# Performance work log

Measured on AMD Instinct MI355X. Metric: run time of the kernel, lower is better.

Reference implementation:

```python
import jax, jax.numpy as jnp
import numpy as np

N_NODES = 50000


def setup_inputs() -> dict:
    key = jax.random.key(0)
    ks = jax.random.split(key, 10)
    E = 800000
    x = jax.random.normal(ks[0], (N_NODES, 256), dtype=jnp.float32)
    src = jax.random.randint(ks[1], (E,), 0, N_NODES, dtype=jnp.int32)
    dst = jax.random.randint(ks[2], (E,), 0, N_NODES, dtype=jnp.int32)
    w = jax.random.uniform(ks[3], (E,), dtype=jnp.float32)
    W1 = jax.random.normal(ks[4], (256, 128), dtype=jnp.float32) / np.sqrt(256)
    b1 = jnp.zeros((128,), dtype=jnp.float32)
    W2 = jax.random.normal(ks[5], (128, 128), dtype=jnp.float32) / np.sqrt(128)
    b2 = jnp.zeros((128,), dtype=jnp.float32)
    W3 = jax.random.normal(ks[6], (128, 64), dtype=jnp.float32) / np.sqrt(128)
    b3 = jnp.zeros((64,), dtype=jnp.float32)
    return {"x": x, "src": src, "dst": dst, "w": w,
            "W1": W1, "b1": b1, "W2": W2, "b2": b2, "W3": W3, "b3": b3}


def _graph_conv(x, src, dst, w, W, b):
    # dense projection then edge-weighted gather-multiply-scatter-sum
    h = x @ W + b                              # [N, d_out]
    msgs = h[src] * w[:, None]                 # [E, d_out] per-edge messages
    return jax.ops.segment_sum(msgs, dst, num_segments=N_NODES)


def reference(x, src, dst, w, W1, b1, W2, b2, W3, b3):
    h = _graph_conv(x, src, dst, w, W1, b1)
    h = jax.nn.relu(h)
    h = _graph_conv(h, src, dst, w, W2, b2)
    h = jax.nn.relu(h)
    h = _graph_conv(h, src, dst, w, W3, b3)
    return h
```

## Files before the change

### kernel.cpp

```cpp
#include <hip/hip_runtime.h>
#include <hip/hip_bf16.h>

#define N_NODES 50000
#define BSHIFT  6
#define BSIZE   64
#define NBUCK   ((N_NODES + BSIZE - 1) / BSIZE)
#define BIN_BLOCKS 512

using short8  = __attribute__((ext_vector_type(8))) short;
using short4v = __attribute__((ext_vector_type(4))) short;
using floatx4 = __attribute__((ext_vector_type(4))) float;

__device__ inline short f32_to_bf16_bits(float f) {
    __hip_bfloat16 h = __float2bfloat16(f);
    return *reinterpret_cast<short*>(&h);
}

template<int K, int N, bool A_F32>
__global__ __launch_bounds__(256) void mfma_gemm(const void* __restrict__ Araw,
                                                 const short* __restrict__ WTf,
                                                 const float* __restrict__ bias,
                                                 short* __restrict__ C, int M)
{
    constexpr int KS = K / 32;
    constexpr int CT = N / 32;
    constexpr int LK = K + 8;

    __shared__ __align__(16) short As[64][LK];

    const int tid  = threadIdx.x;
    const int wave = tid >> 6;
    const int lane = tid & 63;
    const int l15  = lane & 15;
    const int lk   = (lane >> 4) * 8;
    const int wr   = wave >> 1;
    const int wc   = wave & 1;
    const int r0   = blockIdx.x * 64;

    if (A_F32) {
        const float* Af = (const float*)Araw;
#pragma unroll
        for (int it = 0; it < 64 * (K / 4) / 256; ++it) {
            const int idx = it * 256 + tid;
            const int row = idx / (K / 4);
            const int c4  = idx % (K / 4);
            const int gr  = min(r0 + row, M - 1);
            const float4 v = *reinterpret_cast<const float4*>(&Af[(size_t)gr * K + c4 * 4]);
            short4v s;
            s[0] = f32_to_bf16_bits(v.x); s[1] = f32_to_bf16_bits(v.y);
            s[2] = f32_to_bf16_bits(v.z); s[3] = f32_to_bf16_bits(v.w);
            *reinterpret_cast<short4v*>(&As[row][c4 * 4]) = s;
        }
    } else {
        const short* Ab = (const short*)Araw;
#pragma unroll
        for (int it = 0; it < 64 * (K / 8) / 256; ++it) {
            const int idx = it * 256 + tid;
            const int row = idx / (K / 8);
            const int c8  = idx % (K / 8);
            const int gr  = min(r0 + row, M - 1);
            const short8 v = *reinterpret_cast<const short8*>(&Ab[(size_t)gr * K + c8 * 8]);
            *reinterpret_cast<short8*>(&As[row][c8 * 8]) = v;
        }
    }
    __syncthreads();

    float bv[CT];
#pragma unroll
    for (int t = 0; t < CT; ++t) bv[t] = bias[wc * (N / 2) + t * 16 + l15];

    floatx4 acc[2][CT];
#pragma unroll
    for (int rt = 0; rt < 2; ++rt)
#pragma unroll
        for (int t = 0; t < CT; ++t) acc[rt][t] = (floatx4){0.f, 0.f, 0.f, 0.f};

#pragma unroll
    for (int ks = 0; ks < KS; ++ks) {
        short8 b[CT];
#pragma unroll
        for (int t = 0; t < CT; ++t) {
            const int tg = wc * CT + t;
            b[t] = *reinterpret_cast<const short8*>(&WTf[((size_t)(tg * KS + ks) * 64 + lane) * 8]);
        }
        short8 a[2];
#pragma unroll
        for (int rt = 0; rt < 2; ++rt)
            a[rt] = *reinterpret_cast<const short8*>(&As[wr * 32 + rt * 16 + l15][ks * 32 + lk]);
#pragma unroll
        for (int rt = 0; rt < 2; ++rt)
#pragma unroll
            for (int t = 0; t < CT; ++t)
                acc[rt][t] = __builtin_amdgcn_mfma_f32_16x16x32_bf16(a[rt], b[t], acc[rt][t], 0, 0, 0);
    }

    const int rowg = (lane >> 4) * 4;
#pragma unroll
    for (int rt = 0; rt < 2; ++rt)
#pragma unroll
        for (int t = 0; t < CT; ++t)
#pragma unroll
            for (int j = 0; j < 4; ++j) {
                const int gr = r0 + wr * 32 + rt * 16 + rowg + j;
                if (gr < M)
                    C[(size_t)gr * N + wc * (N / 2) + t * 16 + l15] =
                        f32_to_bf16_bits(acc[rt][t][j] + bv[t]);
            }
}

template<int K, int N>
__global__ __launch_bounds__(256) void fused_pull_gemm(const unsigned int* __restrict__ h,
                                                       const int* __restrict__ row_ptr,
                                                       const unsigned int* __restrict__ csr_ew,
                                                       const short* __restrict__ WTf,
                                                       const float* __restrict__ bias,
                                                       short* __restrict__ C, int M)
{
    static_assert(K == 128, "pull input dim is 128");
    constexpr int KS   = K / 32;
    constexpr int LK   = K + 8;
    constexpr int COLT = N / 32;

    __shared__ __align__(16) short As[32][LK];

    const int tid  = threadIdx.x;
    const int wave = tid >> 6;
    const int lane = tid & 63;
    const int q    = lane >> 4;
    const int l16  = lane & 15;
    const int r0   = blockIdx.x * 32;

#pragma unroll
    for (int rnd = 0; rnd < 2; ++rnd) {
        const int lrow = wave * 8 + rnd * 4 + q;
        const int node = r0 + lrow;
        int beg = 0, end = 0;
        if (node < M) { beg = row_ptr[node]; end = row_ptr[node + 1]; }

        float ax[4][4], ay[4][4];
#pragma unroll
        for (int u = 0; u < 4; ++u)
#pragma unroll
            for (int jj = 0; jj < 4; ++jj) { ax[u][jj] = 0.f; ay[u][jj] = 0.f; }

        unsigned ew = (beg + l16 < end) ? csr_ew[beg + l16] : 0u;
        for (int c = beg; c < end; c += 16) {
            const int nidx = c + 16 + l16;
            const unsigned ew_next = (nidx < end) ? csr_ew[nidx] : 0u;
            const int cnt = min(16, end - c);

            for (int j = 0; j < cnt; j += 8) {
                unsigned e[8];
#pragma unroll
                for (int u = 0; u < 8; ++u) {
                    const unsigned v = __shfl(ew, j + u, 16);
                    e[u] = (j + u < cnt) ? v : 0u;
                }
                uint4 p[8];
#pragma unroll
                for (int u = 0; u < 8; ++u)
                    p[u] = *reinterpret_cast<const uint4*>(&h[(size_t)(e[u] >> 16) * 64 + l16 * 4]);
#pragma unroll
                for (int u = 0; u < 8; ++u) {
                    const float wv = __int_as_float(e[u] << 16);
                    const unsigned* pp = reinterpret_cast<const unsigned*>(&p[u]);
#pragma unroll
                    for (int jj = 0; jj < 4; ++jj) {
                        ax[u & 3][jj] = fmaf(__int_as_float(pp[jj] << 16), wv, ax[u & 3][jj]);
                        ay[u & 3][jj] = fmaf(__int_as_float(pp[jj] & 0xffff0000u), wv, ay[u & 3][jj]);
                    }
                }
            }
            ew = ew_next;
        }

        uint4 o;
        unsigned* ov = reinterpret_cast<unsigned*>(&o);
#pragma unroll
        for (int jj = 0; jj < 4; ++jj) {
            float axs = (ax[0][jj] + ax[1][jj]) + (ax[2][jj] + ax[3][jj]);
            float ays = (ay[0][jj] + ay[1][jj]) + (ay[2][jj] + ay[3][jj]);
            axs = fmaxf(axs, 0.f); ays = fmaxf(ays, 0.f);
            ov[jj] = (unsigned)(unsigned short)f32_to_bf16_bits(axs) |
                     ((unsigned)(unsigned short)f32_to_bf16_bits(ays) << 16);
        }
        *reinterpret_cast<uint4*>(&As[lrow][l16 * 8]) = o;
    }
    __syncthreads();

    const int l15 = lane & 15;
    const int lk  = (lane >> 4) * 8;
    const int wr  = wave >> 1;
    const int wc  = wave & 1;

    float bv[COLT];
#pragma unroll
    for (int t = 0; t < COLT; ++t) bv[t] = bias[wc * (N / 2) + t * 16 + l15];

    floatx4 acc[COLT];
#pragma unroll
    for (int t = 0; t < COLT; ++t) acc[t] = (floatx4){0.f, 0.f, 0.f, 0.f};

#pragma unroll
    for (int ks = 0; ks < KS; ++ks) {
        short8 b[COLT];
#pragma unroll
        for (int t = 0; t < COLT; ++t) {
            const int tg = wc * COLT + t;
            b[t] = *reinterpret_cast<const short8*>(&WTf[((size_t)(tg * KS + ks) * 64 + lane) * 8]);
        }
        const short8 a = *reinterpret_cast<const short8*>(&As[wr * 16 + l15][ks * 32 + lk]);
#pragma unroll
        for (int t = 0; t < COLT; ++t)
            acc[t] = __builtin_amdgcn_mfma_f32_16x16x32_bf16(a, b[t], acc[t], 0, 0, 0);
    }

    const int rowg = (lane >> 4) * 4;
#pragma unroll
    for (int t = 0; t < COLT; ++t)
#pragma unroll
        for (int j = 0; j < 4; ++j) {
            const int gr = r0 + wr * 16 + rowg + j;
            if (gr < M)
                C[(size_t)gr * N + wc * (N / 2) + t * 16 + l15] =
                    f32_to_bf16_bits(acc[t][j] + bv[t]);
        }
}

__device__ inline void wt_frag(const float* __restrict__ W, short* __restrict__ out,
                               int K, int N, int u)
{
    const int lane = u & 63;
    const int rest = u >> 6;
    const int KS   = K >> 5;
    const int ks   = rest % KS;
    const int tg   = rest / KS;
    const int n    = tg * 16 + (lane & 15);
    const int kb   = ks * 32 + (lane >> 4) * 8;
    short8 s;
#pragma unroll
    for (int e = 0; e < 8; ++e) s[e] = f32_to_bf16_bits(W[(size_t)(kb + e) * N + n]);
    *reinterpret_cast<short8*>(&out[(size_t)u * 8]) = s;
}

__global__ __launch_bounds__(256) void prep_kernel(const int* __restrict__ dst,
                                                   int* __restrict__ hist_g, int E,
                                                   const float* __restrict__ W1, short* __restrict__ WT1,
                                                   const float* __restrict__ W2, short* __restrict__ WT2,
                                                   const float* __restrict__ W3, short* __restrict__ WT3)
{
    if (blockIdx.x < BIN_BLOCKS) {
        __shared__ int hist[NBUCK];
        for (int t = threadIdx.x; t < NBUCK; t += 256) hist[t] = 0;
        __syncthreads();
        const int chunk = (E + BIN_BLOCKS - 1) / BIN_BLOCKS;
        const int beg = blockIdx.x * chunk;
        const int end = min(beg + chunk, E);
        for (int i = beg + threadIdx.x; i < end; i += 256)
            atomicAdd(&hist[dst[i] >> BSHIFT], 1);
        __syncthreads();
        for (int t = threadIdx.x; t < NBUCK; t += 256)
            hist_g[blockIdx.x * NBUCK + t] = hist[t];
    } else {
        const int u = (blockIdx.x - BIN_BLOCKS) * 256 + threadIdx.x;
        if (u < 4096)             wt_frag(W1, WT1, 256, 128, u);
        else if (u < 4096 + 2048) wt_frag(W2, WT2, 128, 128, u - 4096);
        else if (u < 7168)        wt_frag(W3, WT3, 128, 64,  u - 6144);
    }
}

__global__ __launch_bounds__(BIN_BLOCKS) void bin_scan_blocks(const int* __restrict__ hist_g,
                                                              int* __restrict__ blockbase,
                                                              int* __restrict__ tot)
{
    __shared__ int s[BIN_BLOCKS];
    const int b = blockIdx.x;
    const int t = threadIdx.x;
    const int v = hist_g[t * NBUCK + b];
    s[t] = v;
    __syncthreads();
#pragma unroll
    for (int off = 1; off < BIN_BLOCKS; off <<= 1) {
        const int tmp = (t >= off) ? s[t - off] : 0;
        __syncthreads();
        s[t] += tmp;
        __syncthreads();
    }
    blockbase[t * NBUCK + b] = s[t] - v;
    if (t == BIN_BLOCKS - 1) tot[b] = s[t];
}

__global__ __launch_bounds__(256) void bin_scan_tot(const int* __restrict__ tot,
                                                    int* __restrict__ bucket_base)
{
    __shared__ int psum[256];
    const int t = threadIdx.x;
    int vals[4];
    int s = 0;
#pragma unroll
    for (int j = 0; j < 4; ++j) {
        const int idx = t * 4 + j;
        vals[j] = (idx < NBUCK) ? tot[idx] : 0;
        s += vals[j];
    }
    psum[t] = s;
    __syncthreads();
#pragma unroll
    for (int off = 1; off < 256; off <<= 1) {
        const int tmp = (t >= off) ? psum[t - off] : 0;
        __syncthreads();
        psum[t] += tmp;
        __syncthreads();
    }
    int run = psum[t] - s;
#pragma unroll
    for (int j = 0; j < 4; ++j) {
        const int idx = t * 4 + j;
        if (idx < NBUCK) bucket_base[idx] = run;
        run += vals[j];
    }
    if (t == 255) bucket_base[NBUCK] = run;
}

__global__ __launch_bounds__(256) void bin_write(const int* __restrict__ src,
                                                 const int* __restrict__ dst,
                                                 const float* __restrict__ w,
                                                 const int* __restrict__ blockbase,
                                                 const int* __restrict__ bucket_base,
                                                 int2* __restrict__ tmp, int E)
{
    __shared__ int cur[NBUCK];
    for (int t = threadIdx.x; t < NBUCK; t += 256)
        cur[t] = bucket_base[t] + blockbase[blockIdx.x * NBUCK + t];
    __syncthreads();
    const int chunk = (E + BIN_BLOCKS - 1) / BIN_BLOCKS;
    const int beg = blockIdx.x * chunk;
    const int end = min(beg + chunk, E);
    for (int i = beg + threadIdx.x; i < end; i += 256) {
        const int d = dst[i];
        const int pos = atomicAdd(&cur[d >> BSHIFT], 1);
        tmp[pos] = make_int2((src[i] << BSHIFT) | (d & (BSIZE - 1)), __float_as_int(w[i]));
    }
}

__global__ __launch_bounds__(256) void fine_fill2(const int2* __restrict__ tmp,
                                                  const int* __restrict__ bucket_base,
                                                  unsigned int* __restrict__ csr_ew,
                                                  int* __restrict__ row_ptr)
{
    __shared__ int hist[BSIZE];
    __shared__ int basel[BSIZE];
    const int b    = blockIdx.x;
    const int t    = threadIdx.x;
    const int rbeg = bucket_base[b];
    const int rend = bucket_base[b + 1];

    if (t < BSIZE) hist[t] = 0;
    __syncthreads();
    for (int i = rbeg + t; i < rend; i += 256)
        atomicAdd(&hist[((unsigned)tmp[i].x) & (BSIZE - 1)], 1);
    __syncthreads();

    if (t < BSIZE) {
        const int v = hist[t];
        int inc = v;
#pragma unroll
        for (int off = 1; off < BSIZE; off <<= 1) {
            const int u = __shfl_up(inc, off, 64);
            if (t >= off) inc += u;
        }
        const int excl = rbeg + inc - v;
        basel[t] = excl;
        const int node = (b << BSHIFT) + t;
        if (node < N_NODES) row_ptr[node] = excl;
        if (b == NBUCK - 1 && t == 0) row_ptr[N_NODES] = bucket_base[NBUCK];
    }
    __syncthreads();

    for (int i = rbeg + t; i < rend; i += 256) {
        const int2 e = tmp[i];
        const unsigned ex = (unsigned)e.x;
        const int pos = atomicAdd(&basel[ex & (BSIZE - 1)], 1);
        const unsigned wb = (unsigned short)f32_to_bf16_bits(__int_as_float(e.y));
        csr_ew[pos] = ((ex >> BSHIFT) << 16) | wb;
    }
}

__global__ __launch_bounds__(256) void pull64_bf(const unsigned int* __restrict__ h,
                                                 const int* __restrict__ row_ptr,
                                                 const unsigned int* __restrict__ csr_ew,
                                                 float4* __restrict__ out, int n_nodes)
{
    const int wave = threadIdx.x >> 6;
    const int lane = threadIdx.x & 63;
    const int q    = lane >> 4;
    const int l16  = lane & 15;
    const int node = blockIdx.x * 16 + wave * 4 + q;

    int beg = 0, end = 0;
    if (node < n_nodes) { beg = row_ptr[node]; end = row_ptr[node + 1]; }

    float ax[4][2], ay[4][2];
#pragma unroll
    for (int u = 0; u < 4; ++u)
#pragma unroll
        for (int jj = 0; jj < 2; ++jj) { ax[u][jj] = 0.f; ay[u][jj] = 0.f; }

    unsigned ew = (beg + l16 < end) ? csr_ew[beg + l16] : 0u;
    for (int c = beg; c < end; c += 16) {
        const int nidx = c + 16 + l16;
        const unsigned ew_next = (nidx < end) ? csr_ew[nidx] : 0u;
        const int cnt = min(16, end - c);

        for (int j = 0; j < cnt; j += 8) {
            unsigned e[8];
#pragma unroll
            for (int u = 0; u < 8; ++u) {
                const unsigned v = __shfl(ew, j + u, 16);
                e[u] = (j + u < cnt) ? v : 0u;
            }
            uint2 p[8];
#pragma unroll
            for (int u = 0; u < 8; ++u)
                p[u] = *reinterpret_cast<const uint2*>(&h[(size_t)(e[u] >> 16) * 32 + l16 * 2]);
#pragma unroll
            for (int u = 0; u < 8; ++u) {
                const float wv = __int_as_float(e[u] << 16);
                ax[u & 3][0] = fmaf(__int_as_float(p[u].x << 16), wv, ax[u & 3][0]);
                ay[u & 3][0] = fmaf(__int_as_float(p[u].x & 0xffff0000u), wv, ay[u & 3][0]);
                ax[u & 3][1] = fmaf(__int_as_float(p[u].y << 16), wv, ax[u & 3][1]);
                ay[u & 3][1] = fmaf(__int_as_float(p[u].y & 0xffff0000u), wv, ay[u & 3][1]);
            }
        }
        ew = ew_next;
    }

    if (node < n_nodes) {
        float4 o;
        o.x = (ax[0][0] + ax[1][0]) + (ax[2][0] + ax[3][0]);
        o.y = (ay[0][0] + ay[1][0]) + (ay[2][0] + ay[3][0]);
        o.z = (ax[0][1] + ax[1][1]) + (ax[2][1] + ax[3][1]);
        o.w = (ay[0][1] + ay[1][1]) + (ay[2][1] + ay[3][1]);
        out[(size_t)node * 16 + l16] = o;
    }
}

extern "C" void kernel_launch(void* const* d_in, const int* in_sizes, int n_in,
                              void* d_out, int out_size, void* d_ws, size_t ws_size,
                              hipStream_t stream)
{
    const float* x   = (const float*)d_in[0];
    const int*   src = (const int*)  d_in[1];
    const int*   dst = (const int*)  d_in[2];
    const float* w   = (const float*)d_in[3];
    const float* W1  = (const float*)d_in[4];
    const float* b1  = (const float*)d_in[5];
    const float* W2  = (const float*)d_in[6];
    const float* b2  = (const float*)d_in[7];
    const float* W3  = (const float*)d_in[8];
    const float* b3  = (const float*)d_in[9];

    const int E = in_sizes[1];
    const int M = N_NODES;

    short* hA  = (short*)d_ws;
    short* hB  = hA + (size_t)M * 128;
    short* WT1 = hB + (size_t)M * 128;
    short* WT2 = WT1 + 128 * 256;
    short* WT3 = WT2 + 128 * 128;
    unsigned int* csr_ew = (unsigned int*)(WT3 + 64 * 128);
    int2*  tmp_ew      = (int2*)(csr_ew + ((E + 1) & ~1));
    int*   row_ptr     = (int*)(tmp_ew + E);
    int*   hist_g      = row_ptr + 50048;
    int*   blockbase   = hist_g + 401408;
    int*   bucket_base = blockbase + 401408;
    int*   tot         = bucket_base + 1024;

    prep_kernel<<<BIN_BLOCKS + 28, 256, 0, stream>>>(dst, hist_g, E, W1, WT1, W2, WT2, W3, WT3);
    bin_scan_blocks<<<NBUCK, BIN_BLOCKS, 0, stream>>>(hist_g, blockbase, tot);
    bin_scan_tot<<<1, 256, 0, stream>>>(tot, bucket_base);
    bin_write<<<BIN_BLOCKS, 256, 0, stream>>>(src, dst, w, blockbase, bucket_base, tmp_ew, E);
    fine_fill2<<<NBUCK, 256, 0, stream>>>(tmp_ew, bucket_base, csr_ew, row_ptr);

    mfma_gemm<256, 128, true><<<(M + 63) / 64, 256, 0, stream>>>(x, WT1, b1, hA, M);

    const int fb = (M + 31) / 32;
    fused_pull_gemm<128, 128><<<fb, 256, 0, stream>>>((const unsigned int*)hA, row_ptr, csr_ew,
                                                      WT2, b2, hB, M);
    fused_pull_gemm<128, 64><<<fb, 256, 0, stream>>>((const unsigned int*)hB, row_ptr, csr_ew,
                                                     WT3, b3, hA, M);
    pull64_bf<<<(M + 15) / 16, 256, 0, stream>>>((const unsigned int*)hA, row_ptr, csr_ew,
                                                 (float4*)d_out, M);
}
```

Before: 135.7 us.

## Merge bucket scan with first GEMM and fold total scan into bin_write

The per-bucket block scan and the first layer's x@W1 GEMM now share one launch: the low block indices do the scan and the rest do the GEMM, now with 512 threads as 8 waves each covering 16 rows. The small single-block scan of bucket totals is folded into every bin_write block, which recomputes it redundantly and block 0 writes bucket_base. This removes two kernel launches and lets the independent GEMM overlap the scan work. In exchange, each bin_write block repeats the scan, and the GEMM blocks use a wider, 512-thread shape.

```diff
diff --git a/kernel.cpp b/kernel.cpp
--- a/kernel.cpp
+++ b/kernel.cpp
@@ -16,18 +16,41 @@
     return *reinterpret_cast<short*>(&h);
 }
 
-template<int K, int N, bool A_F32>
-__global__ __launch_bounds__(256) void mfma_gemm(const void* __restrict__ Araw,
-                                                 const short* __restrict__ WTf,
-                                                 const float* __restrict__ bias,
-                                                 short* __restrict__ C, int M)
-{
+__global__ __launch_bounds__(512) void scan_gemm1(const int* __restrict__ hist_g,
+                                                  int* __restrict__ blockbase,
+                                                  int* __restrict__ tot,
+                                                  const float* __restrict__ x,
+                                                  const short* __restrict__ WTf,
+                                                  const float* __restrict__ bias,
+                                                  short* __restrict__ C, int M)
+{
+    if (blockIdx.x < NBUCK) {
+        __shared__ int s[BIN_BLOCKS];
+        const int b = blockIdx.x;
+        const int t = threadIdx.x;
+        const int v = hist_g[t * NBUCK + b];
+        s[t] = v;
+        __syncthreads();
+#pragma unroll
+        for (int off = 1; off < BIN_BLOCKS; off <<= 1) {
+            const int tmp = (t >= off) ? s[t - off] : 0;
+            __syncthreads();
+            s[t] += tmp;
+            __syncthreads();
+        }
+        blockbase[t * NBUCK + b] = s[t] - v;
+        if (t == BIN_BLOCKS - 1) tot[b] = s[t];
+        return;
+    }
+
+    constexpr int K  = 256;
     constexpr int KS = K / 32;
-    constexpr int CT = N / 32;
     constexpr int LK = K + 8;
 
     __shared__ __align__(16) short As[64][LK];
 
+    const int bid  = blockIdx.x - NBUCK;
+    const int r0   = bid * 64;
     const int tid  = threadIdx.x;
     const int wave = tid >> 6;
     const int lane = tid & 63;
@@ -35,77 +58,53 @@
     const int lk   = (lane >> 4) * 8;
     const int wr   = wave >> 1;
     const int wc   = wave & 1;
-    const int r0   = blockIdx.x * 64;
-
-    if (A_F32) {
-        const float* Af = (const float*)Araw;
-#pragma unroll
-        for (int it = 0; it < 64 * (K / 4) / 256; ++it) {
-            const int idx = it * 256 + tid;
-            const int row = idx / (K / 4);
-            const int c4  = idx % (K / 4);
-            const int gr  = min(r0 + row, M - 1);
-            const float4 v = *reinterpret_cast<const float4*>(&Af[(size_t)gr * K + c4 * 4]);
-            short4v s;
-            s[0] = f32_to_bf16_bits(v.x); s[1] = f32_to_bf16_bits(v.y);
-            s[2] = f32_to_bf16_bits(v.z); s[3] = f32_to_bf16_bits(v.w);
-            *reinterpret_cast<short4v*>(&As[row][c4 * 4]) = s;
-        }
-    } else {
-        const short* Ab = (const short*)Araw;
-#pragma unroll
-        for (int it = 0; it < 64 * (K / 8) / 256; ++it) {
-            const int idx = it * 256 + tid;
-            const int row = idx / (K / 8);
-            const int c8  = idx % (K / 8);
-            const int gr  = min(r0 + row, M - 1);
-            const short8 v = *reinterpret_cast<const short8*>(&Ab[(size_t)gr * K + c8 * 8]);
-            *reinterpret_cast<short8*>(&As[row][c8 * 8]) = v;
-        }
-    }
-    __syncthreads();
-
-    float bv[CT];
-#pragma unroll
-    for (int t = 0; t < CT; ++t) bv[t] = bias[wc * (N / 2) + t * 16 + l15];
-
-    floatx4 acc[2][CT];
-#pragma unroll
-    for (int rt = 0; rt < 2; ++rt)
-#pragma unroll
-        for (int t = 0; t < CT; ++t) acc[rt][t] = (floatx4){0.f, 0.f, 0.f, 0.f};
+
+#pragma unroll
+    for (int it = 0; it < 8; ++it) {
+        const int idx = it * 512 + tid;
+        const int row = idx >> 6;
+        const int c4  = idx & 63;
+        const int gr  = min(r0 + row, M - 1);
+        const float4 v = *reinterpret_cast<const float4*>(&x[(size_t)gr * K + c4 * 4]);
+        short4v sv;
+        sv[0] = f32_to_bf16_bits(v.x); sv[1] = f32_to_bf16_bits(v.y);
+        sv[2] = f32_to_bf16_bits(v.z); sv[3] = f32_to_bf16_bits(v.w);
+        *reinterpret_cast<short4v*>(&As[row][c4 * 4]) = sv;
+    }
+    __syncthreads();
+
+    float bv[4];
+#pragma unroll
+    for (int t = 0; t < 4; ++t) bv[t] = bias[wc * 64 + t * 16 + l15];
+
+    floatx4 acc[4];
+#pragma unroll
+    for (int t = 0; t < 4; ++t) acc[t] = (floatx4){0.f, 0.f, 0.f, 0.f};
 
 #pragma unroll
     for (int ks = 0; ks < KS; ++ks) {
-        short8 b[CT];
-#pragma unroll
-        for (int t = 0; t < CT; ++t) {
-            const int tg = wc * CT + t;
+        short8 b[4];
+#pragma unroll
+        for (int t = 0; t < 4; ++t) {
+            const int tg = wc * 4 + t;
             b[t] = *reinterpret_cast<const short8*>(&WTf[((size_t)(tg * KS + ks) * 64 + lane) * 8]);
         }
-        short8 a[2];
-#pragma unroll
-        for (int rt = 0; rt < 2; ++rt)
-            a[rt] = *reinterpret_cast<const short8*>(&As[wr * 32 + rt * 16 + l15][ks * 32 + lk]);
-#pragma unroll
-        for (int rt = 0; rt < 2; ++rt)
-#pragma unroll
-            for (int t = 0; t < CT; ++t)
-                acc[rt][t] = __builtin_amdgcn_mfma_f32_16x16x32_bf16(a[rt], b[t], acc[rt][t], 0, 0, 0);
+        const short8 a = *reinterpret_cast<const short8*>(&As[wr * 16 + l15][ks * 32 + lk]);
+#pragma unroll
+        for (int t = 0; t < 4; ++t)
+            acc[t] = __builtin_amdgcn_mfma_f32_16x16x32_bf16(a, b[t], acc[t], 0, 0, 0);
     }
 
     const int rowg = (lane >> 4) * 4;
 #pragma unroll
-    for (int rt = 0; rt < 2; ++rt)
-#pragma unroll
-        for (int t = 0; t < CT; ++t)
-#pragma unroll
-            for (int j = 0; j < 4; ++j) {
-                const int gr = r0 + wr * 32 + rt * 16 + rowg + j;
-                if (gr < M)
-                    C[(size_t)gr * N + wc * (N / 2) + t * 16 + l15] =
-                        f32_to_bf16_bits(acc[rt][t][j] + bv[t]);
-            }
+    for (int t = 0; t < 4; ++t)
+#pragma unroll
+        for (int j = 0; j < 4; ++j) {
+            const int gr = r0 + wr * 16 + rowg + j;
+            if (gr < M)
+                C[(size_t)gr * 128 + wc * 64 + t * 16 + l15] =
+                    f32_to_bf16_bits(acc[t][j] + bv[t]);
+        }
 }
 
 template<int K, int N>
@@ -269,74 +268,52 @@
     }
 }
 
-__global__ __launch_bounds__(BIN_BLOCKS) void bin_scan_blocks(const int* __restrict__ hist_g,
-                                                              int* __restrict__ blockbase,
-                                                              int* __restrict__ tot)
-{
-    __shared__ int s[BIN_BLOCKS];
-    const int b = blockIdx.x;
-    const int t = threadIdx.x;
-    const int v = hist_g[t * NBUCK + b];
-    s[t] = v;
-    __syncthreads();
-#pragma unroll
-    for (int off = 1; off < BIN_BLOCKS; off <<= 1) {
-        const int tmp = (t >= off) ? s[t - off] : 0;
-        __syncthreads();
-        s[t] += tmp;
-        __syncthreads();
-    }
-    blockbase[t * NBUCK + b] = s[t] - v;
-    if (t == BIN_BLOCKS - 1) tot[b] = s[t];
-}
-
-__global__ __launch_bounds__(256) void bin_scan_tot(const int* __restrict__ tot,
-                                                    int* __restrict__ bucket_base)
-{
-    __shared__ int psum[256];
-    const int t = threadIdx.x;
-    int vals[4];
-    int s = 0;
-#pragma unroll
-    for (int j = 0; j < 4; ++j) {
-        const int idx = t * 4 + j;
-        vals[j] = (idx < NBUCK) ? tot[idx] : 0;
-        s += vals[j];
-    }
-    psum[t] = s;
-    __syncthreads();
-#pragma unroll
-    for (int off = 1; off < 256; off <<= 1) {
-        const int tmp = (t >= off) ? psum[t - off] : 0;
-        __syncthreads();
-        psum[t] += tmp;
-        __syncthreads();
-    }
-    int run = psum[t] - s;
-#pragma unroll
-    for (int j = 0; j < 4; ++j) {
-        const int idx = t * 4 + j;
-        if (idx < NBUCK) bucket_base[idx] = run;
-        run += vals[j];
-    }
-    if (t == 255) bucket_base[NBUCK] = run;
-}
-
 __global__ __launch_bounds__(256) void bin_write(const int* __restrict__ src,
                                                  const int* __restrict__ dst,
                                                  const float* __restrict__ w,
                                                  const int* __restrict__ blockbase,
-                                                 const int* __restrict__ bucket_base,
+                                                 const int* __restrict__ tot,
+                                                 int* __restrict__ bucket_base_out,
                                                  int2* __restrict__ tmp, int E)
 {
     __shared__ int cur[NBUCK];
-    for (int t = threadIdx.x; t < NBUCK; t += 256)
-        cur[t] = bucket_base[t] + blockbase[blockIdx.x * NBUCK + t];
-    __syncthreads();
+    __shared__ int psum[256];
+    const int t = threadIdx.x;
+
+    int vals[4];
+    int sacc = 0;
+#pragma unroll
+    for (int j = 0; j < 4; ++j) {
+        const int idx = t * 4 + j;
+        vals[j] = (idx < NBUCK) ? tot[idx] : 0;
+        sacc += vals[j];
+    }
+    psum[t] = sacc;
+    __syncthreads();
+#pragma unroll
+    for (int off = 1; off < 256; off <<= 1) {
+        const int tmpv = (t >= off) ? psum[t - off] : 0;
+        __syncthreads();
+        psum[t] += tmpv;
+        __syncthreads();
+    }
+    int run = psum[t] - sacc;
+#pragma unroll
+    for (int j = 0; j < 4; ++j) {
+        const int idx = t * 4 + j;
+        if (idx < NBUCK) {
+            cur[idx] = run + blockbase[blockIdx.x * NBUCK + idx];
+            if (blockIdx.x == 0) bucket_base_out[idx] = run;
+        }
+        run += vals[j];
+    }
+    if (blockIdx.x == 0 && t == 255) bucket_base_out[NBUCK] = run;
+    __syncthreads();
+
     const int chunk = (E + BIN_BLOCKS - 1) / BIN_BLOCKS;
     const int beg = blockIdx.x * chunk;
     const int end = min(beg + chunk, E);
-    for (int i = beg + threadIdx.x; i < end; i += 256) {
+    for (int i = beg + t; i < end; i += 256) {
         const int d = dst[i];
         const int pos = atomicAdd(&cur[d >> BSHIFT], 1);
         tmp[pos] = make_int2((src[i] << BSHIFT) | (d & (BSIZE - 1)), __float_as_int(w[i]));
@@ -477,12 +454,13 @@
     int*   tot         = bucket_base + 1024;
 
     prep_kernel<<<BIN_BLOCKS + 28, 256, 0, stream>>>(dst, hist_g, E, W1, WT1, W2, WT2, W3, WT3);
-    bin_scan_blocks<<<NBUCK, BIN_BLOCKS, 0, stream>>>(hist_g, blockbase, tot);
-    bin_scan_tot<<<1, 256, 0, stream>>>(tot, bucket_base);
-    bin_write<<<BIN_BLOCKS, 256, 0, stream>>>(src, dst, w, blockbase, bucket_base, tmp_ew, E);
+
+    scan_gemm1<<<NBUCK + (M + 63) / 64, 512, 0, stream>>>(hist_g, blockbase, tot,
+                                                          x, WT1, b1, hA, M);
+
+    bin_write<<<BIN_BLOCKS, 256, 0, stream>>>(src, dst, w, blockbase, tot, bucket_base, tmp_ew, E);
+
     fine_fill2<<<NBUCK, 256, 0, stream>>>(tmp_ew, bucket_base, csr_ew, row_ptr);
-
-    mfma_gemm<256, 128, true><<<(M + 63) / 64, 256, 0, stream>>>(x, WT1, b1, hA, M);
 
     const int fb = (M + 31) / 32;
     fused_pull_gemm<128, 128><<<fb, 256, 0, stream>>>((const unsigned int*)hA, row_ptr, csr_ew,
```

Measured after the change: 135.2 us. No clear change (-0.4%).
